# Kernel tuning notes

Measured on AMD Instinct MI355X. Metric: run time of the kernel, lower is better.

## Reference

```python
import jax, jax.numpy as jnp
import numpy as np

N_DRUG = 10000
N_DIS = 10000
IN_UNITS = 256
N_EDGES = 1000000


def setup_inputs() -> dict:
    key = jax.random.key(0)
    ks = jax.random.split(key, 10)
    # Kaiming-uniform-ish init like torch Linear defaults
    def lin_w(k, fan_in, fan_out):
        bound = 1.0 / np.sqrt(fan_in)
        return jax.random.uniform(k, (fan_in, fan_out), jnp.float32, -bound, bound)
    return {
        "drug_feat": jax.random.normal(ks[0], (N_DRUG, IN_UNITS), jnp.float32),
        "dis_feat": jax.random.normal(ks[1], (N_DIS, IN_UNITS), jnp.float32),
        "src_idx": jax.random.randint(ks[2], (N_EDGES,), 0, N_DRUG, jnp.int64),
        "dst_idx": jax.random.randint(ks[3], (N_EDGES,), 0, N_DIS, jnp.int64),
        "W1": lin_w(ks[4], 2 * IN_UNITS, 128),
        "b1": jnp.zeros((128,), jnp.float32),
        "W2": lin_w(ks[5], 128, 64),
        "b2": jnp.zeros((64,), jnp.float32),
        "W3": lin_w(ks[6], 64, 1),
        "b3": jnp.zeros((1,), jnp.float32),
    }


def reference(drug_feat, dis_feat, src_idx, dst_idx, W1, b1, W2, b2, W3, b3):
    # apply_edges: gather src (drug) and dst (disease) features, concat -> [E, 2*in_units]
    m = jnp.concatenate([drug_feat[src_idx], dis_feat[dst_idx]], axis=1)
    # 3-layer MLP (dropout = identity in eval)
    h = jax.nn.relu(m @ W1 + b1)
    h = jax.nn.relu(h @ W2 + b2)
    out = h @ W3 + b3  # [E, 1]
    return out
```

## Files before the change

kernel.cpp:

```cpp
#include <hip/hip_runtime.h>
#include <hip/hip_bf16.h>

#define IN_UNITS 256
#define H1 128
#define H2 64

typedef __attribute__((ext_vector_type(8))) short bf16x8;
typedef __attribute__((ext_vector_type(4))) float f32x4;

union BV {
    uint4 u;
    __hip_bfloat162 h[4];
    bf16x8 v;
};

static __device__ __forceinline__ unsigned short bfbits(__hip_bfloat16 b) {
    union { __hip_bfloat16 b; unsigned short u; } c; c.b = b; return c.u;
}

__global__ __launch_bounds__(256) void pack_w2_kernel(
    const float* __restrict__ W2, uint4* __restrict__ w2pack)
{
    int item = blockIdx.x * 256 + threadIdx.x;
    int f = item >> 6, l = item & 63;
    int ks = f >> 2, nt = f & 3;
    int row0 = ks * 32 + (l >> 4) * 8;
    int col  = nt * 16 + (l & 15);
    unsigned short h[8];
    #pragma unroll
    for (int j = 0; j < 8; ++j)
        h[j] = bfbits(__float2bfloat16(W2[(size_t)(row0 + j) * H2 + col]));
    uint4 v;
    v.x = (unsigned)h[0] | ((unsigned)h[1] << 16);
    v.y = (unsigned)h[2] | ((unsigned)h[3] << 16);
    v.z = (unsigned)h[4] | ((unsigned)h[5] << 16);
    v.w = (unsigned)h[6] | ((unsigned)h[7] << 16);
    w2pack[item] = v;
}

__global__ __launch_bounds__(256) void pack_w1_kernel(
    const float* __restrict__ W1, uint4* __restrict__ w1pack)
{
    int idx = blockIdx.x * 256 + threadIdx.x;
    int l = idx & 63, fr = idx >> 6;
    int hl = fr & 1, ntc = (fr >> 1) & 7, ks = (fr >> 4) & 7, side = fr >> 7;
    int row0 = side * IN_UNITS + ks * 32 + (l >> 4) * 8;
    int col  = ntc * 16 + (l & 15);
    unsigned short h[8];
    #pragma unroll
    for (int j = 0; j < 8; ++j) {
        float x = W1[(size_t)(row0 + j) * H1 + col];
        __hip_bfloat16 hi = __float2bfloat16(x);
        __hip_bfloat16 val = hi;
        if (hl) val = __float2bfloat16(x - __bfloat162float(hi));
        h[j] = bfbits(val);
    }
    uint4 v;
    v.x = (unsigned)h[0] | ((unsigned)h[1] << 16);
    v.y = (unsigned)h[2] | ((unsigned)h[3] << 16);
    v.z = (unsigned)h[4] | ((unsigned)h[5] << 16);
    v.w = (unsigned)h[6] | ((unsigned)h[7] << 16);
    w1pack[idx] = v;
}

__global__ __launch_bounds__(256) void proj_kernel(
    const float* __restrict__ drug_feat, const float* __restrict__ dis_feat,
    const uint4* __restrict__ w1pack, const float* __restrict__ b1,
    unsigned short* __restrict__ drug_bf, unsigned short* __restrict__ dis_bf,
    int mtiles, int n_rows)
{
    int lane = threadIdx.x & 63, wave = threadIdx.x >> 6;
    int task = blockIdx.x * 4 + wave;
    int side = task >= 2 * mtiles;
    int t2 = task - side * 2 * mtiles;
    int mtile = t2 >> 1, ch = t2 & 1;
    const float* feat = side ? dis_feat : drug_feat;
    unsigned short* outb = side ? dis_bf : drug_bf;
    int r0 = mtile * 16;
    int kb = (lane >> 4) * 8;
    int row = r0 + (lane & 15);
    if (row >= n_rows) row = n_rows - 1;

    f32x4 acc[4];
    #pragma unroll
    for (int nt = 0; nt < 4; ++nt) acc[nt] = (f32x4){0.f, 0.f, 0.f, 0.f};

    const uint4* wp = w1pack + lane;

    #pragma unroll
    for (int ks = 0; ks < 8; ++ks) {
        const float* ap = feat + (size_t)row * IN_UNITS + ks * 32 + kb;
        float4 x0 = *(const float4*)ap;
        float4 x1 = *(const float4*)(ap + 4);
        float xs[8] = {x0.x, x0.y, x0.z, x0.w, x1.x, x1.y, x1.z, x1.w};
        BV ahi, alo;
        #pragma unroll
        for (int p = 0; p < 4; ++p) {
            float2 pr = make_float2(xs[2 * p], xs[2 * p + 1]);
            __hip_bfloat162 hp = __float22bfloat162_rn(pr);
            ahi.h[p] = hp;
            float2 lo = make_float2(xs[2 * p]     - __bfloat162float(hp.x),
                                    xs[2 * p + 1] - __bfloat162float(hp.y));
            alo.h[p] = __float22bfloat162_rn(lo);
        }
        int fbase = (side << 7) | (ks << 4) | (ch << 3);
        #pragma unroll
        for (int nt = 0; nt < 4; ++nt) {
            BV bhi, blo;
            bhi.u = wp[(size_t)((fbase | (nt << 1)) | 0) * 64];
            blo.u = wp[(size_t)((fbase | (nt << 1)) | 1) * 64];
            acc[nt] = __builtin_amdgcn_mfma_f32_16x16x32_bf16(ahi.v, bhi.v, acc[nt], 0, 0, 0);
            acc[nt] = __builtin_amdgcn_mfma_f32_16x16x32_bf16(alo.v, bhi.v, acc[nt], 0, 0, 0);
            acc[nt] = __builtin_amdgcn_mfma_f32_16x16x32_bf16(ahi.v, blo.v, acc[nt], 0, 0, 0);
        }
    }

    #pragma unroll
    for (int nt = 0; nt < 4; ++nt) {
        int col = ch * 64 + nt * 16 + (lane & 15);
        float bb = side ? b1[col] : 0.f;
        #pragma unroll
        for (int r = 0; r < 4; ++r) {
            int rr = r0 + (lane >> 4) * 4 + r;
            if (rr < n_rows)
                outb[(size_t)rr * H1 + col] = bfbits(__float2bfloat16(acc[nt][r] + bb));
        }
    }
}

__global__ __launch_bounds__(256) void edge_kernel(
    const unsigned short* __restrict__ drug_bf, const unsigned short* __restrict__ dis_bf,
    const int* __restrict__ src_idx, const int* __restrict__ dst_idx,
    const uint4* __restrict__ w2pack, const float* __restrict__ b2,
    const float* __restrict__ W3, const float* __restrict__ b3,
    float* __restrict__ out, int n_edges)
{
    int lane = threadIdx.x & 63;
    int wave = threadIdx.x >> 6;
    long e0 = ((long)blockIdx.x * 4 + wave) * 32;
    if (e0 >= n_edges) return;

    bf16x8 bfrag[4][4];
    {
        const uint4* p = w2pack + lane;
        #pragma unroll
        for (int ks = 0; ks < 4; ++ks)
            #pragma unroll
            for (int nt = 0; nt < 4; ++nt) {
                BV c; c.u = p[(size_t)(ks * 4 + nt) * 64];
                bfrag[ks][nt] = c.v;
            }
    }

    float b2v[4], w3v[4];
    #pragma unroll
    for (int nt = 0; nt < 4; ++nt) {
        int col = (lane & 15) + nt * 16;
        b2v[nt] = b2[col];
        w3v[nt] = W3[col];
    }
    float b3v = b3[0];

    f32x4 acc[2][4];
    #pragma unroll
    for (int mt = 0; mt < 2; ++mt)
        #pragma unroll
        for (int nt = 0; nt < 4; ++nt)
            acc[mt][nt] = (f32x4){0.f, 0.f, 0.f, 0.f};

    int kb = (lane >> 4) * 8;
    __hip_bfloat162 z2 = __float22bfloat162_rn(make_float2(0.f, 0.f));

    #pragma unroll
    for (int mt = 0; mt < 2; ++mt) {
        long em = e0 + mt * 16 + (lane & 15);
        if (em >= n_edges) em = n_edges - 1;
        int s = src_idx[em];
        int d = dst_idx[em];
        const uint4* dp = (const uint4*)(drug_bf + (size_t)s * H1 + kb);
        const uint4* pp = (const uint4*)(dis_bf  + (size_t)d * H1 + kb);

        bf16x8 af[4];
        #pragma unroll
        for (int ks = 0; ks < 4; ++ks) {
            BV a, c, r;
            a.u = dp[ks * 4];
            c.u = pp[ks * 4];
            #pragma unroll
            for (int j = 0; j < 4; ++j)
                r.h[j] = __hmax2(__hadd2(a.h[j], c.h[j]), z2);
            af[ks] = r.v;
        }

        #pragma unroll
        for (int ks = 0; ks < 4; ++ks)
            #pragma unroll
            for (int nt = 0; nt < 4; ++nt)
                acc[mt][nt] = __builtin_amdgcn_mfma_f32_16x16x32_bf16(
                    af[ks], bfrag[ks][nt], acc[mt][nt], 0, 0, 0);
    }

    #pragma unroll
    for (int mt = 0; mt < 2; ++mt) {
        float part[4];
        #pragma unroll
        for (int r = 0; r < 4; ++r) {
            float p = 0.f;
            #pragma unroll
            for (int nt = 0; nt < 4; ++nt)
                p += fmaxf(acc[mt][nt][r] + b2v[nt], 0.f) * w3v[nt];
            part[r] = p;
        }
        #pragma unroll
        for (int off = 1; off <= 8; off <<= 1)
            #pragma unroll
            for (int r = 0; r < 4; ++r)
                part[r] += __shfl_xor(part[r], off, 64);
        if ((lane & 15) == 0) {
            #pragma unroll
            for (int r = 0; r < 4; ++r) {
                long e = e0 + mt * 16 + (lane >> 4) * 4 + r;
                if (e < n_edges) out[e] = part[r] + b3v;
            }
        }
    }
}

extern "C" void kernel_launch(void* const* d_in, const int* in_sizes, int n_in,
                              void* d_out, int out_size, void* d_ws, size_t ws_size,
                              hipStream_t stream) {
    const float* drug_feat = (const float*)d_in[0];
    const float* dis_feat  = (const float*)d_in[1];
    const int*   src_idx   = (const int*)d_in[2];
    const int*   dst_idx   = (const int*)d_in[3];
    const float* W1 = (const float*)d_in[4];
    const float* b1 = (const float*)d_in[5];
    const float* W2 = (const float*)d_in[6];
    const float* b2 = (const float*)d_in[7];
    const float* W3 = (const float*)d_in[8];
    const float* b3 = (const float*)d_in[9];
    float* out = (float*)d_out;

    int n_edges = in_sizes[2];
    int n_drug = in_sizes[0] / IN_UNITS;

    uint4* w2pack = (uint4*)d_ws;
    uint4* w1pack = (uint4*)((char*)d_ws + 16 * 1024);
    unsigned short* drug_bf = (unsigned short*)((char*)d_ws + (16 + 256) * 1024);
    unsigned short* dis_bf  = drug_bf + (size_t)n_drug * H1;

    pack_w2_kernel<<<4, 256, 0, stream>>>(W2, w2pack);
    pack_w1_kernel<<<64, 256, 0, stream>>>(W1, w1pack);

    int mtiles = (n_drug + 15) / 16;
    proj_kernel<<<mtiles, 256, 0, stream>>>(
        drug_feat, dis_feat, w1pack, b1, drug_bf, dis_bf, mtiles, n_drug);

    int edge_blocks = (n_edges + 127) / 128;
    edge_kernel<<<edge_blocks, 256, 0, stream>>>(
        drug_bf, dis_bf, src_idx, dst_idx, w2pack, b2, W3, b3, out, n_edges);
}
```

Baseline: 176.8 us.

## Stage weights in LDS, hoist edge gathers, and merge pack kernels

Merges the two weight-pack kernels into one launch. The projection kernel now stages each block's W1 fragment slice in shared memory, and each block handles one side and one column half across four row tiles. The edge kernel issues all gather loads for both edge tiles up front before staging W2 in shared memory, which gives more memory-level parallelism. Occupancy hints are added to the launch bounds. Costs include LDS usage, 64KB per proj block, and a block-wide barrier. The edge kernel's early-return guard for out-of-range waves is removed and replaced by index clamping.

Measured after the change: 166.6 us. -5.8%, faster.

```diff
diff --git a/kernel.cpp b/kernel.cpp
--- a/kernel.cpp
+++ b/kernel.cpp
@@ -8,72 +8,79 @@
 typedef __attribute__((ext_vector_type(8))) short bf16x8;
 typedef __attribute__((ext_vector_type(4))) float f32x4;
 
-union BV {
-    uint4 u;
-    __hip_bfloat162 h[4];
-    bf16x8 v;
-};
+union BV { uint4 u; __hip_bfloat162 h[4]; bf16x8 v; };
 
 static __device__ __forceinline__ unsigned short bfbits(__hip_bfloat16 b) {
     union { __hip_bfloat16 b; unsigned short u; } c; c.b = b; return c.u;
 }
 
-__global__ __launch_bounds__(256) void pack_w2_kernel(
-    const float* __restrict__ W2, uint4* __restrict__ w2pack)
+__global__ __launch_bounds__(256) void pack_kernel(
+    const float* __restrict__ W1, const float* __restrict__ W2,
+    uint4* __restrict__ w1pack, uint4* __restrict__ w2pack)
 {
-    int item = blockIdx.x * 256 + threadIdx.x;
-    int f = item >> 6, l = item & 63;
-    int ks = f >> 2, nt = f & 3;
-    int row0 = ks * 32 + (l >> 4) * 8;
-    int col  = nt * 16 + (l & 15);
-    unsigned short h[8];
-    #pragma unroll
-    for (int j = 0; j < 8; ++j)
-        h[j] = bfbits(__float2bfloat16(W2[(size_t)(row0 + j) * H2 + col]));
-    uint4 v;
-    v.x = (unsigned)h[0] | ((unsigned)h[1] << 16);
-    v.y = (unsigned)h[2] | ((unsigned)h[3] << 16);
-    v.z = (unsigned)h[4] | ((unsigned)h[5] << 16);
-    v.w = (unsigned)h[6] | ((unsigned)h[7] << 16);
-    w2pack[item] = v;
-}
-
-__global__ __launch_bounds__(256) void pack_w1_kernel(
-    const float* __restrict__ W1, uint4* __restrict__ w1pack)
-{
-    int idx = blockIdx.x * 256 + threadIdx.x;
-    int l = idx & 63, fr = idx >> 6;
-    int hl = fr & 1, ntc = (fr >> 1) & 7, ks = (fr >> 4) & 7, side = fr >> 7;
-    int row0 = side * IN_UNITS + ks * 32 + (l >> 4) * 8;
-    int col  = ntc * 16 + (l & 15);
-    unsigned short h[8];
-    #pragma unroll
-    for (int j = 0; j < 8; ++j) {
-        float x = W1[(size_t)(row0 + j) * H1 + col];
-        __hip_bfloat16 hi = __float2bfloat16(x);
-        __hip_bfloat16 val = hi;
-        if (hl) val = __float2bfloat16(x - __bfloat162float(hi));
-        h[j] = bfbits(val);
-    }
-    uint4 v;
-    v.x = (unsigned)h[0] | ((unsigned)h[1] << 16);
-    v.y = (unsigned)h[2] | ((unsigned)h[3] << 16);
-    v.z = (unsigned)h[4] | ((unsigned)h[5] << 16);
-    v.w = (unsigned)h[6] | ((unsigned)h[7] << 16);
-    w1pack[idx] = v;
-}
-
-__global__ __launch_bounds__(256) void proj_kernel(
+    int b = blockIdx.x, t = threadIdx.x;
+    if (b < 4) {
+        int item = b * 256 + t;
+        int f = item >> 6, l = item & 63;
+        int ks = f >> 2, nt = f & 3;
+        int row0 = ks * 32 + (l >> 4) * 8;
+        int col  = nt * 16 + (l & 15);
+        unsigned short h[8];
+        #pragma unroll
+        for (int j = 0; j < 8; ++j)
+            h[j] = bfbits(__float2bfloat16(W2[(size_t)(row0 + j) * H2 + col]));
+        uint4 v;
+        v.x = (unsigned)h[0] | ((unsigned)h[1] << 16);
+        v.y = (unsigned)h[2] | ((unsigned)h[3] << 16);
+        v.z = (unsigned)h[4] | ((unsigned)h[5] << 16);
+        v.w = (unsigned)h[6] | ((unsigned)h[7] << 16);
+        w2pack[item] = v;
+    } else {
+        int idx = (b - 4) * 256 + t;
+        int l = idx & 63, fr = idx >> 6;
+        int hl = fr & 1, ntc = (fr >> 1) & 7, ks = (fr >> 4) & 7, side = fr >> 7;
+        int row0 = side * IN_UNITS + ks * 32 + (l >> 4) * 8;
+        int col  = ntc * 16 + (l & 15);
+        unsigned short h[8];
+        #pragma unroll
+        for (int j = 0; j < 8; ++j) {
+            float x = W1[(size_t)(row0 + j) * H1 + col];
+            __hip_bfloat16 hi = __float2bfloat16(x);
+            __hip_bfloat16 val = hi;
+            if (hl) val = __float2bfloat16(x - __bfloat162float(hi));
+            h[j] = bfbits(val);
+        }
+        uint4 v;
+        v.x = (unsigned)h[0] | ((unsigned)h[1] << 16);
+        v.y = (unsigned)h[2] | ((unsigned)h[3] << 16);
+        v.z = (unsigned)h[4] | ((unsigned)h[5] << 16);
+        v.w = (unsigned)h[6] | ((unsigned)h[7] << 16);
+        w1pack[idx] = v;
+    }
+}
+
+__global__ __launch_bounds__(256, 2) void proj_kernel(
     const float* __restrict__ drug_feat, const float* __restrict__ dis_feat,
     const uint4* __restrict__ w1pack, const float* __restrict__ b1,
     unsigned short* __restrict__ drug_bf, unsigned short* __restrict__ dis_bf,
-    int mtiles, int n_rows)
+    int n_rows)
 {
-    int lane = threadIdx.x & 63, wave = threadIdx.x >> 6;
-    int task = blockIdx.x * 4 + wave;
-    int side = task >= 2 * mtiles;
-    int t2 = task - side * 2 * mtiles;
-    int mtile = t2 >> 1, ch = t2 & 1;
+    __shared__ uint4 w1s[4096];
+
+    int t = threadIdx.x, lane = t & 63, wave = t >> 6;
+    int b = blockIdx.x;
+    int side = (b >> 1) & 1, ch = b & 1, group = b >> 2;
+
+    #pragma unroll
+    for (int i = 0; i < 16; ++i) {
+        int li = i * 256 + t;
+        int f_loc = li >> 6, l = li & 63;
+        int f_glob = (side << 7) | ((f_loc >> 3) << 4) | (ch << 3) | (f_loc & 7);
+        w1s[li] = w1pack[(size_t)f_glob * 64 + l];
+    }
+    __syncthreads();
+
+    int mtile = group * 4 + wave;
     const float* feat = side ? dis_feat : drug_feat;
     unsigned short* outb = side ? dis_bf : drug_bf;
     int r0 = mtile * 16;
@@ -84,8 +91,6 @@
     f32x4 acc[4];
     #pragma unroll
     for (int nt = 0; nt < 4; ++nt) acc[nt] = (f32x4){0.f, 0.f, 0.f, 0.f};
-
-    const uint4* wp = w1pack + lane;
 
     #pragma unroll
     for (int ks = 0; ks < 8; ++ks) {
@@ -103,12 +108,11 @@
                                     xs[2 * p + 1] - __bfloat162float(hp.y));
             alo.h[p] = __float22bfloat162_rn(lo);
         }
-        int fbase = (side << 7) | (ks << 4) | (ch << 3);
         #pragma unroll
         for (int nt = 0; nt < 4; ++nt) {
             BV bhi, blo;
-            bhi.u = wp[(size_t)((fbase | (nt << 1)) | 0) * 64];
-            blo.u = wp[(size_t)((fbase | (nt << 1)) | 1) * 64];
+            bhi.u = w1s[(ks * 8 + nt * 2 + 0) * 64 + lane];
+            blo.u = w1s[(ks * 8 + nt * 2 + 1) * 64 + lane];
             acc[nt] = __builtin_amdgcn_mfma_f32_16x16x32_bf16(ahi.v, bhi.v, acc[nt], 0, 0, 0);
             acc[nt] = __builtin_amdgcn_mfma_f32_16x16x32_bf16(alo.v, bhi.v, acc[nt], 0, 0, 0);
             acc[nt] = __builtin_amdgcn_mfma_f32_16x16x32_bf16(ahi.v, blo.v, acc[nt], 0, 0, 0);
@@ -128,29 +132,41 @@
     }
 }
 
-__global__ __launch_bounds__(256) void edge_kernel(
+__global__ __launch_bounds__(256, 3) void edge_kernel(
     const unsigned short* __restrict__ drug_bf, const unsigned short* __restrict__ dis_bf,
     const int* __restrict__ src_idx, const int* __restrict__ dst_idx,
     const uint4* __restrict__ w2pack, const float* __restrict__ b2,
     const float* __restrict__ W3, const float* __restrict__ b3,
     float* __restrict__ out, int n_edges)
 {
-    int lane = threadIdx.x & 63;
-    int wave = threadIdx.x >> 6;
+    __shared__ uint4 w2s[1024];
+
+    int t = threadIdx.x, lane = t & 63, wave = t >> 6;
     long e0 = ((long)blockIdx.x * 4 + wave) * 32;
-    if (e0 >= n_edges) return;
-
-    bf16x8 bfrag[4][4];
-    {
-        const uint4* p = w2pack + lane;
-        #pragma unroll
-        for (int ks = 0; ks < 4; ++ks)
-            #pragma unroll
-            for (int nt = 0; nt < 4; ++nt) {
-                BV c; c.u = p[(size_t)(ks * 4 + nt) * 64];
-                bfrag[ks][nt] = c.v;
-            }
-    }
+    long emax = (long)n_edges - 1;
+
+    long em0 = e0 + (lane & 15);       if (em0 > emax) em0 = emax;
+    long em1 = e0 + 16 + (lane & 15);  if (em1 > emax) em1 = emax;
+    int s0 = src_idx[em0], d0 = dst_idx[em0];
+    int s1 = src_idx[em1], d1 = dst_idx[em1];
+
+    int kb = (lane >> 4) * 8;
+    const uint4* pa0 = (const uint4*)(drug_bf + (size_t)s0 * H1 + kb);
+    const uint4* pc0 = (const uint4*)(dis_bf  + (size_t)d0 * H1 + kb);
+    const uint4* pa1 = (const uint4*)(drug_bf + (size_t)s1 * H1 + kb);
+    const uint4* pc1 = (const uint4*)(dis_bf  + (size_t)d1 * H1 + kb);
+    uint4 ga0[4], gc0[4], ga1[4], gc1[4];
+    #pragma unroll
+    for (int ks = 0; ks < 4; ++ks) {
+        ga0[ks] = pa0[ks * 4];
+        gc0[ks] = pc0[ks * 4];
+        ga1[ks] = pa1[ks * 4];
+        gc1[ks] = pc1[ks * 4];
+    }
+
+    #pragma unroll
+    for (int i = 0; i < 4; ++i) w2s[i * 256 + t] = w2pack[i * 256 + t];
+    __syncthreads();
 
     float b2v[4], w3v[4];
     #pragma unroll
@@ -168,36 +184,24 @@
         for (int nt = 0; nt < 4; ++nt)
             acc[mt][nt] = (f32x4){0.f, 0.f, 0.f, 0.f};
 
-    int kb = (lane >> 4) * 8;
     __hip_bfloat162 z2 = __float22bfloat162_rn(make_float2(0.f, 0.f));
 
     #pragma unroll
-    for (int mt = 0; mt < 2; ++mt) {
-        long em = e0 + mt * 16 + (lane & 15);
-        if (em >= n_edges) em = n_edges - 1;
-        int s = src_idx[em];
-        int d = dst_idx[em];
-        const uint4* dp = (const uint4*)(drug_bf + (size_t)s * H1 + kb);
-        const uint4* pp = (const uint4*)(dis_bf  + (size_t)d * H1 + kb);
-
-        bf16x8 af[4];
-        #pragma unroll
-        for (int ks = 0; ks < 4; ++ks) {
-            BV a, c, r;
-            a.u = dp[ks * 4];
-            c.u = pp[ks * 4];
-            #pragma unroll
-            for (int j = 0; j < 4; ++j)
-                r.h[j] = __hmax2(__hadd2(a.h[j], c.h[j]), z2);
-            af[ks] = r.v;
-        }
-
-        #pragma unroll
-        for (int ks = 0; ks < 4; ++ks)
-            #pragma unroll
-            for (int nt = 0; nt < 4; ++nt)
-                acc[mt][nt] = __builtin_amdgcn_mfma_f32_16x16x32_bf16(
-                    af[ks], bfrag[ks][nt], acc[mt][nt], 0, 0, 0);
+    for (int ks = 0; ks < 4; ++ks) {
+        BV a0, c0, a1, c1, r0v, r1v;
+        a0.u = ga0[ks]; c0.u = gc0[ks];
+        a1.u = ga1[ks]; c1.u = gc1[ks];
+        #pragma unroll
+        for (int j = 0; j < 4; ++j) {
+            r0v.h[j] = __hmax2(__hadd2(a0.h[j], c0.h[j]), z2);
+            r1v.h[j] = __hmax2(__hadd2(a1.h[j], c1.h[j]), z2);
+        }
+        #pragma unroll
+        for (int nt = 0; nt < 4; ++nt) {
+            BV bb; bb.u = w2s[(ks * 4 + nt) * 64 + lane];
+            acc[0][nt] = __builtin_amdgcn_mfma_f32_16x16x32_bf16(r0v.v, bb.v, acc[0][nt], 0, 0, 0);
+            acc[1][nt] = __builtin_amdgcn_mfma_f32_16x16x32_bf16(r1v.v, bb.v, acc[1][nt], 0, 0, 0);
+        }
     }
 
     #pragma unroll
@@ -249,12 +253,11 @@
     unsigned short* drug_bf = (unsigned short*)((char*)d_ws + (16 + 256) * 1024);
     unsigned short* dis_bf  = drug_bf + (size_t)n_drug * H1;
 
-    pack_w2_kernel<<<4, 256, 0, stream>>>(W2, w2pack);
-    pack_w1_kernel<<<64, 256, 0, stream>>>(W1, w1pack);
-
-    int mtiles = (n_drug + 15) / 16;
-    proj_kernel<<<mtiles, 256, 0, stream>>>(
-        drug_feat, dis_feat, w1pack, b1, drug_bf, dis_bf, mtiles, n_drug);
+    pack_kernel<<<68, 256, 0, stream>>>(W1, W2, w1pack, w2pack);
+
+    int groups = (((n_drug + 15) / 16) + 3) / 4;
+    proj_kernel<<<groups * 4, 256, 0, stream>>>(
+        drug_feat, dis_feat, w1pack, b1, drug_bf, dis_bf, n_drug);
 
     int edge_blocks = (n_edges + 127) / 128;
     edge_kernel<<<edge_blocks, 256, 0, stream>>>(
```
